# Kernel optimization log

Hardware: AMD Instinct MI355X
Metric: run time of the kernel (lower is better)

Reference implementation:

```python
import jax, jax.numpy as jnp
import numpy as np

NUM_HEADS = 32
NUM_KV_HEADS = 8
HEAD_DIM = 128
ROPE_THETA = 10000.0
NEG_INF = -1e9


def _rope_cos_sin(position_ids, head_dim, dtype):
    # inv_freq: [head_dim/2]
    inv_freq = 1.0 / (ROPE_THETA ** (jnp.arange(0, head_dim, 2, dtype=jnp.float32) / head_dim))
    # freqs: [B, S, head_dim/2]
    freqs = position_ids.astype(jnp.float32)[..., None] * inv_freq[None, None, :]
    emb = jnp.concatenate([freqs, freqs], axis=-1)  # [B, S, head_dim]
    return jnp.cos(emb).astype(dtype), jnp.sin(emb).astype(dtype)


def _rotate_half(x):
    x1, x2 = jnp.split(x, 2, axis=-1)
    return jnp.concatenate([-x2, x1], axis=-1)


def setup_inputs() -> dict:
    key = jax.random.key(0)
    k1, k2, k3, k4, k5 = jax.random.split(key, 5)
    B, S, H = 2, 2048, 4096
    scale = 1.0 / np.sqrt(H)
    return {
        "hidden_states": jax.random.normal(k1, (B, S, H), jnp.float32),
        "position_ids": jnp.broadcast_to(jnp.arange(S, dtype=jnp.int32)[None, :], (B, S)),
        "Wq": jax.random.normal(k2, (H, H), jnp.float32) * scale,
        "Wk": jax.random.normal(k3, (NUM_KV_HEADS * HEAD_DIM, H), jnp.float32) * scale,
        "Wv": jax.random.normal(k4, (NUM_KV_HEADS * HEAD_DIM, H), jnp.float32) * scale,
        "Wo": jax.random.normal(k5, (H, H), jnp.float32) * scale,
    }


def reference(hidden_states, position_ids, Wq, Wk, Wv, Wo):
    B, S, H = hidden_states.shape
    dtype = hidden_states.dtype
    n_rep = NUM_HEADS // NUM_KV_HEADS

    # QKV projections (torch Linear: x @ W.T)
    q = (hidden_states @ Wq.T).reshape(B, S, NUM_HEADS, HEAD_DIM).transpose(0, 2, 1, 3)
    k = (hidden_states @ Wk.T).reshape(B, S, NUM_KV_HEADS, HEAD_DIM).transpose(0, 2, 1, 3)
    v = (hidden_states @ Wv.T).reshape(B, S, NUM_KV_HEADS, HEAD_DIM).transpose(0, 2, 1, 3)

    # RoPE (cos/sin broadcast over heads)
    cos, sin = _rope_cos_sin(position_ids, HEAD_DIM, dtype)
    cos, sin = cos[:, None, :, :], sin[:, None, :, :]  # [B,1,S,D]
    q = q * cos + _rotate_half(q) * sin
    k = k * cos + _rotate_half(k) * sin

    # repeat_kv (GQA): [B, KVH, S, D] -> [B, KVH*n_rep, S, D]
    k = jnp.repeat(k, n_rep, axis=1)
    v = jnp.repeat(v, n_rep, axis=1)

    # scaled dot-product attention with causal mask, softmax in fp32
    scores = jnp.einsum('bhqd,bhkd->bhqk', q, k) / np.sqrt(HEAD_DIM)
    causal = jnp.tril(jnp.ones((S, S), dtype=bool))
    scores = jnp.where(causal[None, None, :, :], scores, NEG_INF)
    probs = jax.nn.softmax(scores.astype(jnp.float32), axis=-1).astype(dtype)

    attn = jnp.einsum('bhqk,bhkd->bhqd', probs, v)
    attn = attn.transpose(0, 2, 1, 3).reshape(B, S, H)
    return attn @ Wo.T
```

## Files before the change

### kernel.cpp

```cpp
#include <hip/hip_runtime.h>

#define S_LEN 2048
#define BATCH 2
#define HID 4096
#define NH 32
#define NKV 8
#define DH 128
#define MROWS (BATCH*S_LEN)
#define QKV_N 6144

typedef unsigned short u16;
typedef unsigned int u32;
typedef __bf16 bf16x8 __attribute__((ext_vector_type(8)));
typedef float f32x4 __attribute__((ext_vector_type(4)));
typedef u16 u16x8 __attribute__((ext_vector_type(8)));

__device__ __forceinline__ u16 f2bf(float f) {
  union { float f; u32 u; } v; v.f = f;
  return (u16)((v.u + 0x8000u) >> 16);
}
__device__ __forceinline__ float bf2f(u16 h) {
  union { u32 u; float f; } v; v.u = ((u32)h) << 16;
  return v.f;
}
__device__ __forceinline__ u32 cvtpk(float a, float b) {
  u32 r;
  asm("v_cvt_pk_bf16_f32 %0, %1, %2" : "=v"(r) : "v"(a), "v"(b));
  return r;
}
__device__ __forceinline__ void async16(const void* g, void* l) {
  __builtin_amdgcn_global_load_lds(
      (const __attribute__((address_space(1))) u32*)g,
      (__attribute__((address_space(3))) u32*)l, 16, 0, 0);
}
__device__ __forceinline__ f32x4 mfma16(bf16x8 a, bf16x8 b, f32x4 c) {
  return __builtin_amdgcn_mfma_f32_16x16x32_bf16(a, b, c, 0, 0, 0);
}

#define BAR()    __builtin_amdgcn_s_barrier()
#define LGKM0()  asm volatile("s_waitcnt lgkmcnt(0)" ::: "memory")
#define PRIO(x)  __builtin_amdgcn_s_setprio(x)

__global__ __launch_bounds__(256) void cvt_f32_bf16(const float* __restrict__ in,
                                                    u16* __restrict__ out, int n) {
  int i0 = (blockIdx.x * 256 + threadIdx.x) * 8;
  if (i0 >= n) return;
  float4 a = *(const float4*)(in + i0);
  float4 b = *(const float4*)(in + i0 + 4);
  u16x8 r;
  r[0]=f2bf(a.x); r[1]=f2bf(a.y); r[2]=f2bf(a.z); r[3]=f2bf(a.w);
  r[4]=f2bf(b.x); r[5]=f2bf(b.y); r[6]=f2bf(b.z); r[7]=f2bf(b.w);
  *(u16x8*)(out + i0) = r;
}

template<int MODE>
__global__ __launch_bounds__(512, 2) void gemm256(
    const u16* __restrict__ A, const u16* __restrict__ B, void* __restrict__ Cout,
    int M, int N, int K, int XC, int SR, int SC,
    int kSpan, int nkt, int tileBase, float* p0, float* p1) {
  __shared__ u16 As[2][2][64 * 128];
  __shared__ u16 Bs[2][2][64 * 128];
  const int NKT = nkt;
  int bid = (int)blockIdx.x;
  int tm, tn, half = 0, slot = 0;
  if (MODE == 0) {
    int xcd = bid & 7, l = bid >> 3;
    tm = (xcd / XC) * SR + l / SC;
    tn = (xcd % XC) * SC + l % SC;
  } else {
    int nTN = N >> 8;
    int lin;
    if (MODE == 2) { half = bid >> 7; slot = bid & 127; lin = tileBase + slot; }
    else           { lin = tileBase + bid; }
    tm = lin / nTN; tn = lin - tm * nTN;
  }
  const int koff = (MODE == 2) ? half * kSpan : 0;
  int m0 = tm << 8, n0 = tn << 8;
  int t = threadIdx.x;
  int w = t >> 6, lane = t & 63, lo = lane & 15, hi = lane >> 4;
  int wm = w >> 2, wn = w & 3;
  int rbb = (wn & 1) << 6;

  int srow = (w << 3) + (lane >> 3);
  int scol = (lane & 7) << 3;

  auto stageA = [&](int kt, int buf, int h) {
#pragma unroll
    for (int c2 = 0; c2 < 2; ++c2) {
      int row = (c2 << 6) + srow;
      int col = scol ^ ((row & 7) << 3);
      async16(A + (size_t)(m0 + (h << 7) + row) * K + (kt << 6) + koff + col,
              (char*)&As[buf][h][0] + (c2 << 13) + (w << 10));
    }
  };
  auto stageB = [&](int kt, int buf, int h) {
#pragma unroll
    for (int c2 = 0; c2 < 2; ++c2) {
      int row = (c2 << 6) + srow;
      int col = scol ^ ((row & 7) << 3);
      async16(B + (size_t)(n0 + (h << 7) + row) * K + (kt << 6) + koff + col,
              (char*)&Bs[buf][h][0] + (c2 << 13) + (w << 10));
    }
  };

  const f32x4 fz = {0.f, 0.f, 0.f, 0.f};
  f32x4 acc[8][4];
#pragma unroll
  for (int i = 0; i < 8; ++i)
#pragma unroll
    for (int j = 0; j < 4; ++j) acc[i][j] = fz;
  bf16x8 af[4][2], bf0[2][2], bf1[2][2];

  auto rdA = [&](int c, int halfT, bf16x8 (&dst)[4][2]) {
    const u16* Ab = &As[c][wm][0];
#pragma unroll
    for (int mf = 0; mf < 4; ++mf)
#pragma unroll
      for (int ks = 0; ks < 2; ++ks) {
        int ra = (halfT << 6) + (mf << 4) + lo;
        dst[mf][ks] = *(const bf16x8*)(Ab + (ra << 6) +
                      (((ks << 5) + (hi << 3)) ^ ((ra & 7) << 3)));
      }
  };
  auto rdB = [&](int c, int bfrag, bf16x8 (&dst)[2][2]) {
    const u16* Bb = &Bs[c][wn >> 1][0];
#pragma unroll
    for (int nf = 0; nf < 2; ++nf)
#pragma unroll
      for (int ks = 0; ks < 2; ++ks) {
        int rb = rbb + (bfrag << 5) + (nf << 4) + lo;
        dst[nf][ks] = *(const bf16x8*)(Bb + (rb << 6) +
                      (((ks << 5) + (hi << 3)) ^ ((rb & 7) << 3)));
      }
  };
  auto MM = [&](bf16x8 (&a)[4][2], bf16x8 (&b)[2][2], int mo, int no) {
#pragma unroll
    for (int mf = 0; mf < 4; ++mf)
#pragma unroll
      for (int nf = 0; nf < 2; ++nf)
#pragma unroll
        for (int ks = 0; ks < 2; ++ks)
          acc[mo + mf][no + nf] = mfma16(a[mf][ks], b[nf][ks], acc[mo + mf][no + nf]);
  };

#define VM4()    asm volatile("s_waitcnt vmcnt(4)" ::: "memory")
  stageA(0, 0, 0); stageA(0, 0, 1);
  stageB(0, 0, 0); stageB(0, 0, 1);
  stageB(1, 1, 0); stageB(1, 1, 1);
  VM4();
  BAR();

  const int NT = NKT >> 1;
  for (int it = 0; it < NT; ++it) {
    int e = it << 1, o = e + 1;
    int e2 = (e + 2 >= NKT) ? 0 : e + 2;
    int o2 = (o + 2 >= NKT) ? 1 : o + 2;

    rdA(0, 0, af); rdB(0, 0, bf0);
    stageA(o, 1, 0);
    BAR(); LGKM0(); PRIO(1);
    MM(af, bf0, 0, 0);
    PRIO(0); BAR();

    rdB(0, 1, bf1);
    stageA(o, 1, 1);
    BAR(); LGKM0(); PRIO(1);
    MM(af, bf1, 0, 2);
    PRIO(0); BAR();

    rdA(0, 1, af);
    stageB(e2, 0, 0);
    BAR(); LGKM0(); PRIO(1);
    MM(af, bf1, 4, 2);
    PRIO(0); BAR();

    stageB(e2, 0, 1);
    BAR(); PRIO(1);
    MM(af, bf0, 4, 0);
    PRIO(0); VM4(); BAR();

    rdA(1, 0, af); rdB(1, 0, bf0);
    stageA(e2, 0, 0);
    BAR(); LGKM0(); PRIO(1);
    MM(af, bf0, 0, 0);
    PRIO(0); BAR();

    rdB(1, 1, bf1);
    stageA(e2, 0, 1);
    BAR(); LGKM0(); PRIO(1);
    MM(af, bf1, 0, 2);
    PRIO(0); BAR();

    rdA(1, 1, af);
    stageB(o2, 1, 0);
    BAR(); LGKM0(); PRIO(1);
    MM(af, bf1, 4, 2);
    PRIO(0); BAR();

    stageB(o2, 1, 1);
    BAR(); PRIO(1);
    MM(af, bf0, 4, 0);
    PRIO(0); VM4(); BAR();
  }
#undef VM4

  float* dst = (MODE == 2) ? ((half ? p1 : p0) + (size_t)slot * 65536) : nullptr;
#pragma unroll
  for (int mf = 0; mf < 8; ++mf)
#pragma unroll
    for (int nf = 0; nf < 4; ++nf)
#pragma unroll
      for (int r = 0; r < 4; ++r) {
        int r_l = (wm << 7) + (mf << 4) + (hi << 2) + r;
        int c_l = (wn << 6) + (nf << 4) + lo;
        if (MODE == 2) {
          dst[(size_t)r_l * 256 + c_l] = acc[mf][nf][r];
        } else {
          int row = m0 + r_l, col = n0 + c_l;
          if (MODE == 1) ((u16*)Cout)[(size_t)row * N + col] = f2bf(acc[mf][nf][r]);
          else           ((float*)Cout)[(size_t)row * N + col] = acc[mf][nf][r];
        }
      }
}

__global__ __launch_bounds__(256) void reduce_splitk(const float* __restrict__ p0,
                                                     const float* __restrict__ p1,
                                                     u16* __restrict__ C) {
  int g = blockIdx.x * 256 + threadIdx.x;
  int s = g >> 13;
  int loc = g & 8191;
  int r_l = loc >> 5, c8 = loc & 31;
  int lin = 256 + s;
  int tm = lin / 24, tn = lin - tm * 24;
  size_t off = (size_t)s * 65536 + r_l * 256 + c8 * 8;
  float4 x0 = *(const float4*)(p0 + off);
  float4 x1 = *(const float4*)(p0 + off + 4);
  float4 y0 = *(const float4*)(p1 + off);
  float4 y1 = *(const float4*)(p1 + off + 4);
  u16x8 r;
  r[0]=f2bf(x0.x+y0.x); r[1]=f2bf(x0.y+y0.y); r[2]=f2bf(x0.z+y0.z); r[3]=f2bf(x0.w+y0.w);
  r[4]=f2bf(x1.x+y1.x); r[5]=f2bf(x1.y+y1.y); r[6]=f2bf(x1.z+y1.z); r[7]=f2bf(x1.w+y1.w);
  *(u16x8*)(C + (size_t)(tm * 256 + r_l) * QKV_N + tn * 256 + c8 * 8) = r;
}

__global__ __launch_bounds__(256) void rope_kernel(u16* __restrict__ X,
                                                   const int* __restrict__ pos,
                                                   int ncols, int pitch, float scale) {
  int idx = blockIdx.x * 256 + threadIdx.x;
  int groups = ncols >> 3;
  int m = idx / groups;
  int gi = idx - m * groups;
  if (m >= MROWS) return;
  int head = gi >> 4;
  int d0 = (gi & 15) << 2;
  float p = (float)pos[m];
  u16* base = X + (size_t)m * pitch + head * 128;
  u16 xa[4], xb[4], oa[4], ob[4];
  *(uint2*)xa = *(const uint2*)(base + d0);
  *(uint2*)xb = *(const uint2*)(base + d0 + 64);
#pragma unroll
  for (int i = 0; i < 4; ++i) {
    float j = (float)(d0 + i);
    float inv = __expf(j * -0.14391156516030342f);
    float fr = p * inv;
    float s, c;
    sincosf(fr, &s, &c);
    float x1 = bf2f(xa[i]), x2 = bf2f(xb[i]);
    oa[i] = f2bf((x1 * c - x2 * s) * scale);
    ob[i] = f2bf((x2 * c + x1 * s) * scale);
  }
  *(uint2*)(base + d0) = *(uint2*)oa;
  *(uint2*)(base + d0 + 64) = *(uint2*)ob;
}

__global__ __launch_bounds__(256) void transpose_v(const u16* __restrict__ V,
                                                   u16* __restrict__ Vt) {
  int bid = blockIdx.x;
  int s0 = (bid & 31) << 6;
  int bg = bid >> 5;
  int b = bg >> 3, g = bg & 7;
  __shared__ u16 tile[64][128];
  int t = threadIdx.x;
#pragma unroll
  for (int r = 0; r < 4; ++r) {
    int c = (r << 8) + t;
    int row = c >> 4, cc = c & 15;
    *(uint4*)&tile[row][cc * 8] =
        *(const uint4*)(V + (size_t)(b * S_LEN + s0 + row) * QKV_N + g * 128 + cc * 8);
  }
  __syncthreads();
#pragma unroll
  for (int r = 0; r < 4; ++r) {
    int c = (r << 8) + t;
    int d = c >> 3, cs = c & 7;
    u16 tmp[8];
#pragma unroll
    for (int i = 0; i < 8; ++i) tmp[i] = tile[cs * 8 + i][d];
    *(uint4*)(Vt + ((size_t)bg * 128 + d) * S_LEN + s0 + cs * 8) = *(uint4*)tmp;
  }
}

__global__ __launch_bounds__(256) void attn_kernel(
    const u16* __restrict__ Q, const u16* __restrict__ K,
    const u16* __restrict__ Vt, u16* __restrict__ O) {
  int bid = blockIdx.x;
  int qt = 31 - (bid >> 6);
  int bh = bid & 63;
  int b = bh >> 5, h = bh & 31;
  int g = h >> 2;
  __shared__ u16 Kl[2][64 * 128];
  __shared__ u16 Vl[2][128 * 64];
  __shared__ u16 Pl[4][16 * 72];
  int t = threadIdx.x, w = t >> 6, lane = t & 63, lo = lane & 15, hi = lane >> 4;

  bf16x8 qf[4];
  {
    const u16* qb = Q + (size_t)(b * S_LEN + (qt << 6) + (w << 4) + lo) * QKV_N + h * 128;
#pragma unroll
    for (int kk = 0; kk < 4; ++kk) qf[kk] = *(const bf16x8*)(qb + kk * 32 + hi * 8);
  }
  const f32x4 fz = {0.f, 0.f, 0.f, 0.f};
  f32x4 acc[8];
#pragma unroll
  for (int f = 0; f < 8; ++f) acc[f] = fz;
  float mrun = -1e30f, lrun = 0.f;

  const u16* Kbase = K + (size_t)(b * S_LEN) * QKV_N + g * 128;
  const u16* Vbase = Vt + (size_t)((b << 3) + g) * 128 * S_LEN;

  auto stageKV = [&](int tile, int buf) {
    int s0 = tile << 6;
#pragma unroll
    for (int r = 0; r < 4; ++r) {
      int c = (r << 8) + (w << 6) + lane;
      int row = c >> 4, cc = c & 15;
      int src = cc ^ (row & 7);
      async16(Kbase + (size_t)(s0 + row) * QKV_N + src * 8,
              (char*)&Kl[buf][0] + (r << 12) + (w << 10));
    }
#pragma unroll
    for (int r = 0; r < 4; ++r) {
      int c = (r << 8) + (w << 6) + lane;
      int row = c >> 3, cc = c & 7;
      int src = cc ^ (row & 7);
      async16(Vbase + (size_t)row * S_LEN + s0 + src * 8,
              (char*)&Vl[buf][0] + (r << 12) + (w << 10));
    }
  };

  int ntiles = qt + 1;
  stageKV(0, 0);
  __syncthreads();

  for (int tile = 0; tile < ntiles; ++tile) {
    int c = tile & 1;
    if (tile + 1 < ntiles) stageKV(tile + 1, c ^ 1);

    f32x4 sf[4];
#pragma unroll
    for (int j = 0; j < 4; ++j) {
      f32x4 sv = fz;
#pragma unroll
      for (int kk = 0; kk < 4; ++kk) {
        int row = (j << 4) + lo;
        int ch = ((kk << 2) + hi) ^ (row & 7);
        bf16x8 kf = *(const bf16x8*)(&Kl[c][0] + row * 128 + ch * 8);
        sv = __builtin_amdgcn_mfma_f32_16x16x32_bf16(kf, qf[kk], sv, 0, 0, 0);
      }
      sf[j] = sv;
    }
    if (tile == qt) {
      int q_rel = (w << 4) + lo;
#pragma unroll
      for (int j = 0; j < 4; ++j)
#pragma unroll
        for (int r = 0; r < 4; ++r)
          if (((j << 4) + (hi << 2) + r) > q_rel) sf[j][r] = -1e9f;
    }
    float pmax = sf[0][0];
#pragma unroll
    for (int j = 0; j < 4; ++j)
#pragma unroll
      for (int r = 0; r < 4; ++r) pmax = fmaxf(pmax, sf[j][r]);
    pmax = fmaxf(pmax, __shfl_xor(pmax, 16, 64));
    pmax = fmaxf(pmax, __shfl_xor(pmax, 32, 64));
    if (__any(pmax > mrun + 8.f)) {
      float mn = fmaxf(mrun, pmax);
      float fsc = __expf(mrun - mn);
      mrun = mn;
      lrun *= fsc;
#pragma unroll
      for (int f = 0; f < 8; ++f)
#pragma unroll
        for (int r = 0; r < 4; ++r) acc[f][r] *= fsc;
    }
    float psum = 0.f;
#pragma unroll
    for (int j = 0; j < 4; ++j)
#pragma unroll
      for (int r = 0; r < 4; ++r) {
        float p = __expf(sf[j][r] - mrun);
        sf[j][r] = p;
        psum += p;
      }
    psum += __shfl_xor(psum, 16, 64);
    psum += __shfl_xor(psum, 32, 64);
    lrun += psum;

#pragma unroll
    for (int j = 0; j < 4; ++j) {
      uint2 pk;
      pk.x = cvtpk(sf[j][0], sf[j][1]);
      pk.y = cvtpk(sf[j][2], sf[j][3]);
      *(uint2*)&Pl[w][lo * 72 + (j << 4) + (hi << 2)] = pk;
    }
#pragma unroll
    for (int kk = 0; kk < 2; ++kk) {
      bf16x8 pf = *(const bf16x8*)&Pl[w][lo * 72 + (kk << 5) + (hi << 3)];
#pragma unroll
      for (int f = 0; f < 8; ++f) {
        int vrow = (f << 4) + lo;
        int phys = ((kk << 2) + hi) ^ (vrow & 7);
        bf16x8 vf = *(const bf16x8*)(&Vl[c][0] + vrow * 64 + phys * 8);
        acc[f] = __builtin_amdgcn_mfma_f32_16x16x32_bf16(vf, pf, acc[f], 0, 0, 0);
      }
    }
    __syncthreads();
  }

  float rl = 1.0f / lrun;
#pragma unroll
  for (int half = 0; half < 2; ++half) {
#pragma unroll
    for (int f2 = 0; f2 < 4; ++f2) {
      int f = (half << 2) + f2;
      uint2 pk;
      pk.x = cvtpk(acc[f][0] * rl, acc[f][1] * rl);
      pk.y = cvtpk(acc[f][2] * rl, acc[f][3] * rl);
      *(uint2*)&Pl[w][lo * 72 + (f2 << 4) + (hi << 2)] = pk;
    }
#pragma unroll
    for (int it = 0; it < 2; ++it) {
      int rowq = (lane >> 3) + (it << 3);
      int c8 = lane & 7;
      uint4 val = *(const uint4*)&Pl[w][rowq * 72 + c8 * 8];
      *(uint4*)(O + (size_t)(b * S_LEN + (qt << 6) + (w << 4) + rowq) * 4096 +
                h * 128 + (half << 6) + c8 * 8) = val;
    }
  }
}

extern "C" void kernel_launch(void* const* d_in, const int* in_sizes, int n_in,
                              void* d_out, int out_size, void* d_ws, size_t ws_size,
                              hipStream_t stream) {
  const float* hidden = (const float*)d_in[0];
  const int* pos = (const int*)d_in[1];
  const float* Wq = (const float*)d_in[2];
  const float* Wk = (const float*)d_in[3];
  const float* Wv = (const float*)d_in[4];
  const float* Wo = (const float*)d_in[5];
  float* out = (float*)d_out;

  u16* hb   = (u16*)d_ws;
  u16* wqb  = hb   + 16777216;
  u16* wkb  = wqb  + 16777216;
  u16* wvb  = wkb  + 4194304;
  u16* wob  = wvb  + 4194304;
  u16* QKVb = wob  + 16777216;
  u16* Vtb  = QKVb + 25165824;
  u16* Ob   = Vtb  + 4194304;
  float* part0 = (float*)wob;
  float* part1 = (float*)Ob;

  cvt_f32_bf16<<<8192, 256, 0, stream>>>(hidden, hb, 16777216);
  cvt_f32_bf16<<<8192, 256, 0, stream>>>(Wq, wqb, 16777216);
  cvt_f32_bf16<<<2048, 256, 0, stream>>>(Wk, wkb, 4194304);
  cvt_f32_bf16<<<2048, 256, 0, stream>>>(Wv, wvb, 4194304);

  gemm256<1><<<256, 512, 0, stream>>>(hb, wqb, QKVb, 4096, QKV_N, 4096,
                                      0, 0, 0, 0, 64, 0, nullptr, nullptr);
  gemm256<2><<<256, 512, 0, stream>>>(hb, wqb, QKVb, 4096, QKV_N, 4096,
                                      0, 0, 0, 2048, 32, 256, part0, part1);
  reduce_splitk<<<4096, 256, 0, stream>>>(part0, part1, QKVb);

  cvt_f32_bf16<<<8192, 256, 0, stream>>>(Wo, wob, 16777216);

  rope_kernel<<<8192, 256, 0, stream>>>(QKVb, pos, 4096, QKV_N, 0.08838834764831845f);
  rope_kernel<<<2048, 256, 0, stream>>>(QKVb + 4096, pos, 1024, QKV_N, 1.0f);

  transpose_v<<<512, 256, 0, stream>>>(QKVb + 5120, Vtb);

  attn_kernel<<<2048, 256, 0, stream>>>(QKVb, QKVb + 4096, Vtb, Ob);

  gemm256<0><<<256, 512, 0, stream>>>(Ob, wob, out, 4096, 4096, 4096,
                                      2, 4, 8, 0, 64, 0, nullptr, nullptr);
}
```

Before: 516.2 us.

## Use 128-row query blocks with 8 waves sharing single-buffered K/V tiles

The attention kernel now handles 128 query rows per block with 8 waves instead of 64 rows with 4 waves. Each K/V tile staged in LDS is reused by twice as many waves, halving global K/V traffic per query. The double-buffered prefetch is replaced by load-then-barrier single buffering, which lowers LDS use but exposes load latency unless other resident blocks hide it. The causal mask now uses global indices, so the first four waves run a fully masked extra tile on the diagonal.

```diff
diff --git a/kernel.cpp b/kernel.cpp
--- a/kernel.cpp
+++ b/kernel.cpp
@@ -300,24 +300,24 @@
   }
 }
 
-__global__ __launch_bounds__(256) void attn_kernel(
+__global__ __launch_bounds__(512) void attn_kernel(
     const u16* __restrict__ Q, const u16* __restrict__ K,
     const u16* __restrict__ Vt, u16* __restrict__ O) {
   int bid = blockIdx.x;
-  int qt = 31 - (bid >> 6);
+  int qb = 15 - (bid >> 6);
   int bh = bid & 63;
   int b = bh >> 5, h = bh & 31;
   int g = h >> 2;
-  __shared__ u16 Kl[2][64 * 128];
-  __shared__ u16 Vl[2][128 * 64];
-  __shared__ u16 Pl[4][16 * 72];
+  __shared__ u16 Kl[64 * 128];
+  __shared__ u16 Vl[128 * 64];
+  __shared__ u16 Pl[8][16 * 72];
   int t = threadIdx.x, w = t >> 6, lane = t & 63, lo = lane & 15, hi = lane >> 4;
 
   bf16x8 qf[4];
   {
-    const u16* qb = Q + (size_t)(b * S_LEN + (qt << 6) + (w << 4) + lo) * QKV_N + h * 128;
-#pragma unroll
-    for (int kk = 0; kk < 4; ++kk) qf[kk] = *(const bf16x8*)(qb + kk * 32 + hi * 8);
+    const u16* qb_ = Q + (size_t)(b * S_LEN + (qb << 7) + (w << 4) + lo) * QKV_N + h * 128;
+#pragma unroll
+    for (int kk = 0; kk < 4; ++kk) qf[kk] = *(const bf16x8*)(qb_ + kk * 32 + hi * 8);
   }
   const f32x4 fz = {0.f, 0.f, 0.f, 0.f};
   f32x4 acc[8];
@@ -328,33 +328,32 @@
   const u16* Kbase = K + (size_t)(b * S_LEN) * QKV_N + g * 128;
   const u16* Vbase = Vt + (size_t)((b << 3) + g) * 128 * S_LEN;
 
-  auto stageKV = [&](int tile, int buf) {
+  auto stageKV = [&](int tile) {
     int s0 = tile << 6;
 #pragma unroll
-    for (int r = 0; r < 4; ++r) {
-      int c = (r << 8) + (w << 6) + lane;
+    for (int r = 0; r < 2; ++r) {
+      int c = (r << 9) + t;
       int row = c >> 4, cc = c & 15;
       int src = cc ^ (row & 7);
       async16(Kbase + (size_t)(s0 + row) * QKV_N + src * 8,
-              (char*)&Kl[buf][0] + (r << 12) + (w << 10));
-    }
-#pragma unroll
-    for (int r = 0; r < 4; ++r) {
-      int c = (r << 8) + (w << 6) + lane;
+              (char*)Kl + (r << 13) + (w << 10));
+    }
+#pragma unroll
+    for (int r = 0; r < 2; ++r) {
+      int c = (r << 9) + t;
       int row = c >> 3, cc = c & 7;
       int src = cc ^ (row & 7);
       async16(Vbase + (size_t)row * S_LEN + s0 + src * 8,
-              (char*)&Vl[buf][0] + (r << 12) + (w << 10));
-    }
-  };
-
-  int ntiles = qt + 1;
-  stageKV(0, 0);
-  __syncthreads();
+              (char*)Vl + (r << 13) + (w << 10));
+    }
+  };
+
+  int ntiles = (qb + 1) << 1;
+  int q_glob = (qb << 7) + (w << 4) + lo;
 
   for (int tile = 0; tile < ntiles; ++tile) {
-    int c = tile & 1;
-    if (tile + 1 < ntiles) stageKV(tile + 1, c ^ 1);
+    stageKV(tile);
+    __syncthreads();
 
     f32x4 sf[4];
 #pragma unroll
@@ -364,18 +363,18 @@
       for (int kk = 0; kk < 4; ++kk) {
         int row = (j << 4) + lo;
         int ch = ((kk << 2) + hi) ^ (row & 7);
-        bf16x8 kf = *(const bf16x8*)(&Kl[c][0] + row * 128 + ch * 8);
+        bf16x8 kf = *(const bf16x8*)(Kl + row * 128 + ch * 8);
         sv = __builtin_amdgcn_mfma_f32_16x16x32_bf16(kf, qf[kk], sv, 0, 0, 0);
       }
       sf[j] = sv;
     }
-    if (tile == qt) {
-      int q_rel = (w << 4) + lo;
+    if (tile >= (qb << 1)) {
+      int kbase = tile << 6;
 #pragma unroll
       for (int j = 0; j < 4; ++j)
 #pragma unroll
         for (int r = 0; r < 4; ++r)
-          if (((j << 4) + (hi << 2) + r) > q_rel) sf[j][r] = -1e9f;
+          if ((kbase + (j << 4) + (hi << 2) + r) > q_glob) sf[j][r] = -1e9f;
     }
     float pmax = sf[0][0];
 #pragma unroll
@@ -421,7 +420,7 @@
       for (int f = 0; f < 8; ++f) {
         int vrow = (f << 4) + lo;
         int phys = ((kk << 2) + hi) ^ (vrow & 7);
-        bf16x8 vf = *(const bf16x8*)(&Vl[c][0] + vrow * 64 + phys * 8);
+        bf16x8 vf = *(const bf16x8*)(Vl + vrow * 64 + phys * 8);
         acc[f] = __builtin_amdgcn_mfma_f32_16x16x32_bf16(vf, pf, acc[f], 0, 0, 0);
       }
     }
@@ -444,7 +443,7 @@
       int rowq = (lane >> 3) + (it << 3);
       int c8 = lane & 7;
       uint4 val = *(const uint4*)&Pl[w][rowq * 72 + c8 * 8];
-      *(uint4*)(O + (size_t)(b * S_LEN + (qt << 6) + (w << 4) + rowq) * 4096 +
+      *(uint4*)(O + (size_t)(b * S_LEN + (qb << 7) + (w << 4) + rowq) * 4096 +
                 h * 128 + (half << 6) + c8 * 8) = val;
     }
   }
@@ -490,7 +489,7 @@
 
   transpose_v<<<512, 256, 0, stream>>>(QKVb + 5120, Vtb);
 
-  attn_kernel<<<2048, 256, 0, stream>>>(QKVb, QKVb + 4096, Vtb, Ob);
+  attn_kernel<<<1024, 512, 0, stream>>>(QKVb, QKVb + 4096, Vtb, Ob);
 
   gemm256<0><<<256, 512, 0, stream>>>(Ob, wob, out, 4096, 4096, 4096,
                                       2, 4, 8, 0, 64, 0, nullptr, nullptr);
```

Measured after the change: 496.3 us, median of 3. -3.9%, faster.
